# Performance work log

Measured on AMD Instinct MI355X. Metric: run time of the kernel, lower is better.

## Reference

```python
import jax, jax.numpy as jnp
import numpy as np

B, L, D, P = 2, 1024, 256, 32

def setup_inputs() -> dict:
    key = jax.random.key(0)
    k1, k2, k3, k4, k5 = jax.random.split(key, 5)
    x = jax.random.normal(k1, (B, L, D), dtype=jnp.float32)
    s_in = 1.0 / np.sqrt(D)
    W_phase = jax.random.normal(k2, (D, P), dtype=jnp.float32) * s_in
    b_phase = jax.random.normal(k3, (P,), dtype=jnp.float32) * 0.01
    W_val = jax.random.normal(k4, (D, D), dtype=jnp.float32) * s_in
    b_val = jax.random.normal(k5, (D,), dtype=jnp.float32) * 0.01
    return {"x": x, "W_phase": W_phase, "b_phase": b_phase, "W_val": W_val, "b_val": b_val}

def reference(x, W_phase, b_phase, W_val, b_val):
    # phases: [B, L, P] in (-pi, pi)
    phases = jnp.tanh(x @ W_phase + b_phase) * jnp.float32(np.pi)
    # unit-magnitude complex phasors: [B, L, P]
    phasors = jnp.exp(1j * phases)  # complex64
    # values: [B, L, D]
    values = x @ W_val + b_val
    # bind value vector to each phasor via outer product: [B, L, P, D] complex64
    bound = phasors[..., None] * values[:, :, None, :].astype(jnp.complex64)
    # holographic memory = running sum over sequence position
    memory = jnp.cumsum(bound, axis=1)
    return (memory, phases, phasors)
```

## Files before the change

### kernel.cpp

```cpp
#include <hip/hip_runtime.h>
#include <math.h>

#define B_ 2
#define L_ 1024
#define D_ 256
#define P_ 32
#define NROW (B_*L_)
#define C_ 16
#define CL_ (L_/C_)
#define PIF 3.14159265358979323846f

typedef float nvf4 __attribute__((ext_vector_type(4)));
typedef float nvf2 __attribute__((ext_vector_type(2)));

__global__ __launch_bounds__(256) void k_proj2(
    const float* __restrict__ x, const float* __restrict__ Wp,
    const float* __restrict__ bp, const float* __restrict__ Wv,
    const float* __restrict__ bv, float* __restrict__ values,
    float* __restrict__ phases_out, float* __restrict__ phasor_out,
    int phasorMode)
{
    __shared__ float xs[8 * D_];
    const int tid = threadIdx.x;

    if (blockIdx.x < NROW / 4) {
        const int row0 = blockIdx.x * 4;
        const float4* xg4 = (const float4*)(x + (size_t)row0 * D_);
        ((float4*)xs)[tid] = xg4[tid];
        __syncthreads();

        const int c4 = tid & 63;
        const int r  = tid >> 6;
        const float* xr = xs + r * D_;
        const float4* Wv4 = (const float4*)Wv;
        float4 acc = make_float4(0.f, 0.f, 0.f, 0.f);
        #pragma unroll 8
        for (int k = 0; k < D_; ++k) {
            float4 w = Wv4[k * 64 + c4];
            float xv = xr[k];
            acc.x += xv * w.x; acc.y += xv * w.y;
            acc.z += xv * w.z; acc.w += xv * w.w;
        }
        const float4 b4 = ((const float4*)bv)[c4];
        acc.x += b4.x; acc.y += b4.y; acc.z += b4.z; acc.w += b4.w;
        ((float4*)values)[(size_t)(row0 + r) * 64 + c4] = acc;
    } else {
        const int row0 = (blockIdx.x - NROW / 4) * 8;
        const float4* xg4 = (const float4*)(x + (size_t)row0 * D_);
        ((float4*)xs)[tid]       = xg4[tid];
        ((float4*)xs)[tid + 256] = xg4[tid + 256];
        __syncthreads();

        const int p  = tid & (P_ - 1);
        const int rr = tid >> 5;
        const float* xr = xs + rr * D_;
        float a = 0.f;
        #pragma unroll 8
        for (int k = 0; k < D_; ++k)
            a += xr[k] * Wp[k * P_ + p];
        float ph = tanhf(a + bp[p]) * PIF;
        const int idx = (row0 + rr) * P_ + p;
        phases_out[idx] = ph;
        if (phasorMode == 0) {
            float s, c;
            sincosf(ph, &s, &c);
            ((float2*)phasor_out)[idx] = make_float2(c, s);
        } else if (phasorMode == 1) {
            phasor_out[idx] = cosf(ph);
        }
    }
}

__global__ __launch_bounds__(128) void k_partial(
    const float* __restrict__ values, const float* __restrict__ phases,
    float4* __restrict__ S4)
{
    const int blk = blockIdx.x;
    const int c = blk & (C_ - 1);
    const int p = (blk >> 4) & (P_ - 1);
    const int b = blk >> 9;
    const int tid = threadIdx.x;
    const int l0 = c * CL_;

    __shared__ float2 pc[CL_];
    if (tid < CL_) {
        float ph = phases[(b * L_ + l0 + tid) * P_ + p];
        pc[tid] = make_float2(__cosf(ph), __sinf(ph));
    }
    __syncthreads();

    const float2* v2 = (const float2*)(values + (size_t)(b * L_ + l0) * D_);
    float4 acc = make_float4(0.f, 0.f, 0.f, 0.f);
    #pragma unroll 4
    for (int i = 0; i < CL_; ++i) {
        float2 ph = pc[i];
        float2 v  = v2[i * (D_/2) + tid];
        acc.x += ph.x * v.x;
        acc.y += ph.y * v.x;
        acc.z += ph.x * v.y;
        acc.w += ph.y * v.y;
    }
    S4[((b * P_ + p) * C_ + c) * (D_/2) + tid] = acc;
}

__global__ __launch_bounds__(128) void k_scan(
    const float* __restrict__ values, const float* __restrict__ phases,
    const float4* __restrict__ S4, float* __restrict__ mem, int mode)
{
    const int blk = blockIdx.x;
    const int c = blk & (C_ - 1);
    const int p = (blk >> 4) & (P_ - 1);
    const int b = blk >> 9;
    const int tid = threadIdx.x;
    const int l0 = c * CL_;

    __shared__ float2 pc[CL_];
    if (tid < CL_) {
        float ph = phases[(b * L_ + l0 + tid) * P_ + p];
        pc[tid] = make_float2(__cosf(ph), __sinf(ph));
    }

    float4 carry = make_float4(0.f, 0.f, 0.f, 0.f);
    const float4* Sbase = S4 + (size_t)(b * P_ + p) * C_ * (D_/2) + tid;
    for (int cc = 0; cc < c; ++cc) {
        float4 s = Sbase[cc * (D_/2)];
        carry.x += s.x; carry.y += s.y; carry.z += s.z; carry.w += s.w;
    }
    __syncthreads();

    const float2* v2 = (const float2*)(values + (size_t)(b * L_ + l0) * D_);
    #pragma unroll 4
    for (int i = 0; i < CL_; ++i) {
        float2 ph = pc[i];
        float2 v  = v2[i * (D_/2) + tid];
        carry.x += ph.x * v.x;
        carry.y += ph.y * v.x;
        carry.z += ph.x * v.y;
        carry.w += ph.y * v.y;
        const size_t rowIdx = (size_t)(b * L_ + l0 + i) * P_ + p;
        if (mode == 0) {
            nvf4 cv = { carry.x, carry.y, carry.z, carry.w };
            __builtin_nontemporal_store(cv, (nvf4*)mem + rowIdx * (D_/2) + tid);
        } else {
            nvf2 cv = { carry.x, carry.z };
            __builtin_nontemporal_store(cv, (nvf2*)mem + rowIdx * (D_/2) + tid);
        }
    }
}

__global__ __launch_bounds__(128) void k_scan_rc(
    const float* __restrict__ values, const float* __restrict__ phases,
    float* __restrict__ mem, int mode)
{
    const int blk = blockIdx.x;
    const int c = blk & (C_ - 1);
    const int p = (blk >> 4) & (P_ - 1);
    const int b = blk >> 9;
    const int tid = threadIdx.x;
    const int l0 = c * CL_;

    const float2* vb = (const float2*)(values + (size_t)b * L_ * D_);
    float4 carry = make_float4(0.f, 0.f, 0.f, 0.f);
    for (int l = 0; l < l0; ++l) {
        float ph = phases[(b * L_ + l) * P_ + p];
        float s = __sinf(ph), cs = __cosf(ph);
        float2 v = vb[l * (D_/2) + tid];
        carry.x += cs * v.x; carry.y += s * v.x;
        carry.z += cs * v.y; carry.w += s * v.y;
    }
    for (int i = 0; i < CL_; ++i) {
        const int l = l0 + i;
        float ph = phases[(b * L_ + l) * P_ + p];
        float s = __sinf(ph), cs = __cosf(ph);
        float2 v = vb[l * (D_/2) + tid];
        carry.x += cs * v.x; carry.y += s * v.x;
        carry.z += cs * v.y; carry.w += s * v.y;
        const size_t rowIdx = (size_t)(b * L_ + l) * P_ + p;
        if (mode == 0) ((float4*)mem)[rowIdx * (D_/2) + tid] = carry;
        else ((float2*)mem)[rowIdx * (D_/2) + tid] = make_float2(carry.x, carry.z);
    }
}

extern "C" void kernel_launch(void* const* d_in, const int* in_sizes, int n_in,
                              void* d_out, int out_size, void* d_ws, size_t ws_size,
                              hipStream_t stream) {
    const float* x  = (const float*)d_in[0];
    const float* Wp = (const float*)d_in[1];
    const float* bp = (const float*)d_in[2];
    const float* Wv = (const float*)d_in[3];
    const float* bv = (const float*)d_in[4];
    float* out = (float*)d_out;

    const size_t nMemF = (size_t)2 * B_ * L_ * P_ * D_;
    const size_t nMemR = (size_t)B_ * L_ * P_ * D_;
    const size_t nPh   = (size_t)B_ * L_ * P_;

    int mode; size_t memFloats;
    if ((size_t)out_size >= nMemF + 3 * nPh) { mode = 0; memFloats = nMemF; }
    else                                     { mode = 1; memFloats = nMemR; }
    const bool memFits      = (size_t)out_size >= memFloats;
    const bool phasesInOut  = (size_t)out_size >= memFloats + nPh;
    const bool phasorsInOut =
        (size_t)out_size >= memFloats + nPh + (mode == 0 ? 2 * nPh : nPh);

    const size_t valB = (size_t)B_ * L_ * D_ * sizeof(float);
    const size_t phB  = nPh * sizeof(float);
    const size_t s4B  = (size_t)B_ * P_ * C_ * (D_/2) * sizeof(float4);
    float*  values   = (float*)d_ws;
    float*  phasesWs = (float*)((char*)d_ws + valB);
    float4* S4       = (float4*)((char*)d_ws + valB + phB);

    float* phasesPtr = phasesInOut ? (out + memFloats)
                     : (ws_size >= valB + phB ? phasesWs : nullptr);
    if (phasesPtr == nullptr) return;

    float* phasorPtr = phasorsInOut ? (out + memFloats + nPh) : nullptr;
    const int phasorMode = phasorsInOut ? mode : 2;

    k_proj2<<<NROW / 4 + NROW / 8, 256, 0, stream>>>(
        x, Wp, bp, Wv, bv, values, phasesPtr, phasorPtr, phasorMode);
    if (!memFits) return;

    if (ws_size >= valB + phB + s4B) {
        k_partial<<<B_ * P_ * C_, 128, 0, stream>>>(values, phasesPtr, S4);
        k_scan<<<B_ * P_ * C_, 128, 0, stream>>>(values, phasesPtr, S4, out, mode);
    } else {
        k_scan_rc<<<B_ * P_ * C_, 128, 0, stream>>>(values, phasesPtr, out, mode);
    }
}
```

Before: 118.1 us.

## Fuse projection, chunk partials and scan into one cooperative kernel with grid syncs

Replaces the three launches (projection, partial sums, scan) with one cooperative kernel of 512 blocks that uses grid.sync between phases. Phasors are computed once and stored transposed for the scan, which now uses 8 segments of 128 steps with 256 threads each handling one D column. The value GEMM is split over k across thread groups with a shared-memory reduction. This removes launch gaps and repeated sin/cos work, but relies on every block being co-resident and gives the scan phase fewer, longer blocks.

```diff
diff --git a/kernel.cpp b/kernel.cpp
--- a/kernel.cpp
+++ b/kernel.cpp
@@ -1,19 +1,142 @@
 #include <hip/hip_runtime.h>
+#include <hip/hip_cooperative_groups.h>
 #include <math.h>
+
+namespace cg = cooperative_groups;
 
 #define B_ 2
 #define L_ 1024
 #define D_ 256
 #define P_ 32
 #define NROW (B_*L_)
-#define C_ 16
-#define CL_ (L_/C_)
+#define SEG_ 8
+#define SL_ (L_/SEG_)
 #define PIF 3.14159265358979323846f
 
-typedef float nvf4 __attribute__((ext_vector_type(4)));
 typedef float nvf2 __attribute__((ext_vector_type(2)));
 
-__global__ __launch_bounds__(256) void k_proj2(
+__global__ __launch_bounds__(256, 2) void k_fused(
+    const float* __restrict__ x, const float* __restrict__ Wp,
+    const float* __restrict__ bp, const float* __restrict__ Wv,
+    const float* __restrict__ bv, float* __restrict__ values,
+    float* __restrict__ phases_out, float* __restrict__ phasor_out,
+    float2* __restrict__ phasorT, float2* __restrict__ S2,
+    float* __restrict__ mem, int mode, int phasorMode)
+{
+    cg::grid_group grid = cg::this_grid();
+    __shared__ float smem[5120];
+    const int tid = threadIdx.x;
+    const int blk = blockIdx.x;
+
+    {
+        const int row0 = blk * 4;
+        float*  xsv = smem;
+        float4* red = (float4*)(smem + 1024);
+
+        ((float4*)xsv)[tid] = ((const float4*)(x + (size_t)row0 * D_))[tid];
+        __syncthreads();
+
+        const int q  = tid >> 6;
+        const int c4 = tid & 63;
+        const float4* Wv4 = (const float4*)Wv;
+        float4 acc[4];
+        #pragma unroll
+        for (int r = 0; r < 4; ++r) acc[r] = make_float4(0.f, 0.f, 0.f, 0.f);
+        const int k0 = q * 64;
+        #pragma unroll 4
+        for (int kk = 0; kk < 64; ++kk) {
+            const int k = k0 + kk;
+            float4 w = Wv4[k * 64 + c4];
+            #pragma unroll
+            for (int r = 0; r < 4; ++r) {
+                float xv = xsv[r * D_ + k];
+                acc[r].x += xv * w.x; acc[r].y += xv * w.y;
+                acc[r].z += xv * w.z; acc[r].w += xv * w.w;
+            }
+        }
+        #pragma unroll
+        for (int r = 0; r < 4; ++r) red[(r * 4 + q) * 64 + c4] = acc[r];
+        __syncthreads();
+
+        const int r2 = tid >> 6;
+        float4 s0 = red[(r2 * 4 + 0) * 64 + c4];
+        float4 s1 = red[(r2 * 4 + 1) * 64 + c4];
+        float4 s2 = red[(r2 * 4 + 2) * 64 + c4];
+        float4 s3 = red[(r2 * 4 + 3) * 64 + c4];
+        const float4 b4 = ((const float4*)bv)[c4];
+        float4 vo;
+        vo.x = s0.x + s1.x + s2.x + s3.x + b4.x;
+        vo.y = s0.y + s1.y + s2.y + s3.y + b4.y;
+        vo.z = s0.z + s1.z + s2.z + s3.z + b4.z;
+        vo.w = s0.w + s1.w + s2.w + s3.w + b4.w;
+        ((float4*)values)[(size_t)(row0 + r2) * 64 + c4] = vo;
+
+        if (tid < 4 * P_) {
+            const int rr = tid >> 5;
+            const int p  = tid & (P_ - 1);
+            const float* xr = xsv + rr * D_;
+            float a = 0.f;
+            #pragma unroll 8
+            for (int k = 0; k < D_; ++k)
+                a += xr[k] * Wp[k * P_ + p];
+            float ph = tanhf(a + bp[p]) * PIF;
+            const int row = row0 + rr;
+            const int idx = row * P_ + p;
+            phases_out[idx] = ph;
+            float s, c;
+            sincosf(ph, &s, &c);
+            if (phasorMode == 0)      ((float2*)phasor_out)[idx] = make_float2(c, s);
+            else if (phasorMode == 1) phasor_out[idx] = c;
+            const int b = row >> 10, l = row & (L_ - 1);
+            phasorT[(b * P_ + p) * L_ + l] = make_float2(c, s);
+        }
+    }
+    grid.sync();
+
+    const int b  = blk >> 8;
+    const int p  = (blk >> 3) & (P_ - 1);
+    const int j  = blk & (SEG_ - 1);
+    const int l0 = j * SL_;
+
+    float2* pc = (float2*)smem;
+    if (tid < SL_) pc[tid] = phasorT[(b * P_ + p) * L_ + l0 + tid];
+    __syncthreads();
+
+    const float* vbase = values + (size_t)(b * L_ + l0) * D_ + tid;
+    float2 accp = make_float2(0.f, 0.f);
+    #pragma unroll 8
+    for (int i = 0; i < SL_; ++i) {
+        float  v  = vbase[i * D_];
+        float2 cs = pc[i];
+        accp.x += cs.x * v;
+        accp.y += cs.y * v;
+    }
+    S2[((b * P_ + p) * SEG_ + j) * D_ + tid] = accp;
+    grid.sync();
+
+    float2 carry = make_float2(0.f, 0.f);
+    const float2* Sb = S2 + (size_t)(b * P_ + p) * SEG_ * D_ + tid;
+    for (int jj = 0; jj < j; ++jj) {
+        float2 s = Sb[jj * D_];
+        carry.x += s.x; carry.y += s.y;
+    }
+    #pragma unroll 4
+    for (int i = 0; i < SL_; ++i) {
+        float  v  = vbase[i * D_];
+        float2 cs = pc[i];
+        carry.x += cs.x * v;
+        carry.y += cs.y * v;
+        const size_t rowIdx = (size_t)(b * L_ + l0 + i) * P_ + p;
+        if (mode == 0) {
+            nvf2 cv = { carry.x, carry.y };
+            __builtin_nontemporal_store(cv, (nvf2*)mem + rowIdx * D_ + tid);
+        } else {
+            __builtin_nontemporal_store(carry.x, mem + rowIdx * D_ + tid);
+        }
+    }
+}
+
+__global__ __launch_bounds__(256) void k_proj_pc(
     const float* __restrict__ x, const float* __restrict__ Wp,
     const float* __restrict__ bp, const float* __restrict__ Wv,
     const float* __restrict__ bv, float* __restrict__ values,
@@ -22,19 +145,14 @@
 {
     __shared__ float xs[8 * D_];
     const int tid = threadIdx.x;
-
     if (blockIdx.x < NROW / 4) {
         const int row0 = blockIdx.x * 4;
-        const float4* xg4 = (const float4*)(x + (size_t)row0 * D_);
-        ((float4*)xs)[tid] = xg4[tid];
-        __syncthreads();
-
-        const int c4 = tid & 63;
-        const int r  = tid >> 6;
+        ((float4*)xs)[tid] = ((const float4*)(x + (size_t)row0 * D_))[tid];
+        __syncthreads();
+        const int c4 = tid & 63, r = tid >> 6;
         const float* xr = xs + r * D_;
         const float4* Wv4 = (const float4*)Wv;
         float4 acc = make_float4(0.f, 0.f, 0.f, 0.f);
-        #pragma unroll 8
         for (int k = 0; k < D_; ++k) {
             float4 w = Wv4[k * 64 + c4];
             float xv = xr[k];
@@ -50,101 +168,17 @@
         ((float4*)xs)[tid]       = xg4[tid];
         ((float4*)xs)[tid + 256] = xg4[tid + 256];
         __syncthreads();
-
-        const int p  = tid & (P_ - 1);
-        const int rr = tid >> 5;
+        const int p = tid & (P_ - 1), rr = tid >> 5;
         const float* xr = xs + rr * D_;
         float a = 0.f;
-        #pragma unroll 8
-        for (int k = 0; k < D_; ++k)
-            a += xr[k] * Wp[k * P_ + p];
+        for (int k = 0; k < D_; ++k) a += xr[k] * Wp[k * P_ + p];
         float ph = tanhf(a + bp[p]) * PIF;
         const int idx = (row0 + rr) * P_ + p;
         phases_out[idx] = ph;
-        if (phasorMode == 0) {
-            float s, c;
-            sincosf(ph, &s, &c);
-            ((float2*)phasor_out)[idx] = make_float2(c, s);
-        } else if (phasorMode == 1) {
-            phasor_out[idx] = cosf(ph);
-        }
-    }
-}
-
-__global__ __launch_bounds__(128) void k_partial(
-    const float* __restrict__ values, const float* __restrict__ phases,
-    float4* __restrict__ S4)
-{
-    const int blk = blockIdx.x;
-    const int c = blk & (C_ - 1);
-    const int p = (blk >> 4) & (P_ - 1);
-    const int b = blk >> 9;
-    const int tid = threadIdx.x;
-    const int l0 = c * CL_;
-
-    __shared__ float2 pc[CL_];
-    if (tid < CL_) {
-        float ph = phases[(b * L_ + l0 + tid) * P_ + p];
-        pc[tid] = make_float2(__cosf(ph), __sinf(ph));
-    }
-    __syncthreads();
-
-    const float2* v2 = (const float2*)(values + (size_t)(b * L_ + l0) * D_);
-    float4 acc = make_float4(0.f, 0.f, 0.f, 0.f);
-    #pragma unroll 4
-    for (int i = 0; i < CL_; ++i) {
-        float2 ph = pc[i];
-        float2 v  = v2[i * (D_/2) + tid];
-        acc.x += ph.x * v.x;
-        acc.y += ph.y * v.x;
-        acc.z += ph.x * v.y;
-        acc.w += ph.y * v.y;
-    }
-    S4[((b * P_ + p) * C_ + c) * (D_/2) + tid] = acc;
-}
-
-__global__ __launch_bounds__(128) void k_scan(
-    const float* __restrict__ values, const float* __restrict__ phases,
-    const float4* __restrict__ S4, float* __restrict__ mem, int mode)
-{
-    const int blk = blockIdx.x;
-    const int c = blk & (C_ - 1);
-    const int p = (blk >> 4) & (P_ - 1);
-    const int b = blk >> 9;
-    const int tid = threadIdx.x;
-    const int l0 = c * CL_;
-
-    __shared__ float2 pc[CL_];
-    if (tid < CL_) {
-        float ph = phases[(b * L_ + l0 + tid) * P_ + p];
-        pc[tid] = make_float2(__cosf(ph), __sinf(ph));
-    }
-
-    float4 carry = make_float4(0.f, 0.f, 0.f, 0.f);
-    const float4* Sbase = S4 + (size_t)(b * P_ + p) * C_ * (D_/2) + tid;
-    for (int cc = 0; cc < c; ++cc) {
-        float4 s = Sbase[cc * (D_/2)];
-        carry.x += s.x; carry.y += s.y; carry.z += s.z; carry.w += s.w;
-    }
-    __syncthreads();
-
-    const float2* v2 = (const float2*)(values + (size_t)(b * L_ + l0) * D_);
-    #pragma unroll 4
-    for (int i = 0; i < CL_; ++i) {
-        float2 ph = pc[i];
-        float2 v  = v2[i * (D_/2) + tid];
-        carry.x += ph.x * v.x;
-        carry.y += ph.y * v.x;
-        carry.z += ph.x * v.y;
-        carry.w += ph.y * v.y;
-        const size_t rowIdx = (size_t)(b * L_ + l0 + i) * P_ + p;
-        if (mode == 0) {
-            nvf4 cv = { carry.x, carry.y, carry.z, carry.w };
-            __builtin_nontemporal_store(cv, (nvf4*)mem + rowIdx * (D_/2) + tid);
-        } else {
-            nvf2 cv = { carry.x, carry.z };
-            __builtin_nontemporal_store(cv, (nvf2*)mem + rowIdx * (D_/2) + tid);
-        }
+        float s, c;
+        sincosf(ph, &s, &c);
+        if (phasorMode == 0)      ((float2*)phasor_out)[idx] = make_float2(c, s);
+        else if (phasorMode == 1) phasor_out[idx] = c;
     }
 }
 
@@ -153,31 +187,22 @@
     float* __restrict__ mem, int mode)
 {
     const int blk = blockIdx.x;
-    const int c = blk & (C_ - 1);
-    const int p = (blk >> 4) & (P_ - 1);
-    const int b = blk >> 9;
+    const int c = blk & 15, p = (blk >> 4) & (P_ - 1), b = blk >> 9;
     const int tid = threadIdx.x;
-    const int l0 = c * CL_;
-
+    const int l0 = c * 64;
     const float2* vb = (const float2*)(values + (size_t)b * L_ * D_);
     float4 carry = make_float4(0.f, 0.f, 0.f, 0.f);
-    for (int l = 0; l < l0; ++l) {
+    for (int l = 0; l < l0 + 64; ++l) {
         float ph = phases[(b * L_ + l) * P_ + p];
         float s = __sinf(ph), cs = __cosf(ph);
         float2 v = vb[l * (D_/2) + tid];
         carry.x += cs * v.x; carry.y += s * v.x;
         carry.z += cs * v.y; carry.w += s * v.y;
-    }
-    for (int i = 0; i < CL_; ++i) {
-        const int l = l0 + i;
-        float ph = phases[(b * L_ + l) * P_ + p];
-        float s = __sinf(ph), cs = __cosf(ph);
-        float2 v = vb[l * (D_/2) + tid];
-        carry.x += cs * v.x; carry.y += s * v.x;
-        carry.z += cs * v.y; carry.w += s * v.y;
-        const size_t rowIdx = (size_t)(b * L_ + l) * P_ + p;
-        if (mode == 0) ((float4*)mem)[rowIdx * (D_/2) + tid] = carry;
-        else ((float2*)mem)[rowIdx * (D_/2) + tid] = make_float2(carry.x, carry.z);
+        if (l >= l0) {
+            const size_t rowIdx = (size_t)(b * L_ + l) * P_ + p;
+            if (mode == 0) ((float4*)mem)[rowIdx * (D_/2) + tid] = carry;
+            else ((float2*)mem)[rowIdx * (D_/2) + tid] = make_float2(carry.x, carry.z);
+        }
     }
 }
 
@@ -204,27 +229,34 @@
         (size_t)out_size >= memFloats + nPh + (mode == 0 ? 2 * nPh : nPh);
 
     const size_t valB = (size_t)B_ * L_ * D_ * sizeof(float);
+    const size_t ptB  = (size_t)B_ * P_ * L_ * sizeof(float2);
+    const size_t s2B  = (size_t)B_ * P_ * SEG_ * D_ * sizeof(float2);
     const size_t phB  = nPh * sizeof(float);
-    const size_t s4B  = (size_t)B_ * P_ * C_ * (D_/2) * sizeof(float4);
-    float*  values   = (float*)d_ws;
-    float*  phasesWs = (float*)((char*)d_ws + valB);
-    float4* S4       = (float4*)((char*)d_ws + valB + phB);
+    float*  values  = (float*)d_ws;
+    float2* phasorT = (float2*)((char*)d_ws + valB);
+    float2* S2      = (float2*)((char*)d_ws + valB + ptB);
+    float*  phasesWs = (float*)((char*)d_ws + valB + ptB + s2B);
 
     float* phasesPtr = phasesInOut ? (out + memFloats)
-                     : (ws_size >= valB + phB ? phasesWs : nullptr);
-    if (phasesPtr == nullptr) return;
+                     : (ws_size >= valB + ptB + s2B + phB ? phasesWs
+                     : (ws_size >= phB ? (float*)d_ws : nullptr));
+    if (phasesPtr == nullptr || !memFits) return;
 
     float* phasorPtr = phasorsInOut ? (out + memFloats + nPh) : nullptr;
     const int phasorMode = phasorsInOut ? mode : 2;
 
-    k_proj2<<<NROW / 4 + NROW / 8, 256, 0, stream>>>(
-        x, Wp, bp, Wv, bv, values, phasesPtr, phasorPtr, phasorMode);
-    if (!memFits) return;
-
-    if (ws_size >= valB + phB + s4B) {
-        k_partial<<<B_ * P_ * C_, 128, 0, stream>>>(values, phasesPtr, S4);
-        k_scan<<<B_ * P_ * C_, 128, 0, stream>>>(values, phasesPtr, S4, out, mode);
+    if (ws_size >= valB + ptB + s2B) {
+        void* args[] = {
+            (void*)&x, (void*)&Wp, (void*)&bp, (void*)&Wv, (void*)&bv,
+            (void*)&values, (void*)&phasesPtr, (void*)&phasorPtr,
+            (void*)&phasorT, (void*)&S2, (void*)&out,
+            (void*)&mode, (void*)&phasorMode
+        };
+        hipLaunchCooperativeKernel((void*)k_fused, dim3(NROW / 4), dim3(256),
+                                   args, 0, stream);
     } else {
-        k_scan_rc<<<B_ * P_ * C_, 128, 0, stream>>>(values, phasesPtr, out, mode);
-    }
-}
+        k_proj_pc<<<NROW / 4 + NROW / 8, 256, 0, stream>>>(
+            x, Wp, bp, Wv, bv, values, phasesPtr, phasorPtr, phasorMode);
+        k_scan_rc<<<B_ * P_ * 16, 128, 0, stream>>>(values, phasesPtr, out, mode);
+    }
+}
```

After: 227.6 us. 1.93x slower.
